# Kernel optimization log

Measured on AMD Instinct MI355X. Metric: run time of the kernel, lower is better.

## Reference

```python
import jax, jax.numpy as jnp
import numpy as np

VOCAB = 30
D_MODEL = 512
D_K = 64
D_V = 64
N_HEAD = 8
D_FF = 2048
N_LAYERS = 4
LN_EPS = 1e-5


def _make_pe(max_len, d_model):
    pos = np.arange(max_len, dtype=np.float32)[:, None]
    div = np.exp(np.arange(0, d_model, 2, dtype=np.float32) * (-np.log(10000.0) / d_model))
    pe = np.zeros((max_len, d_model), dtype=np.float32)
    pe[:, 0::2] = np.sin(pos * div)
    pe[:, 1::2] = np.cos(pos * div)
    return jnp.asarray(pe)


def setup_inputs() -> dict:
    key = jax.random.key(0)
    ks = jax.random.split(key, 16)
    B, S = 4, 2048
    s = 0.02
    inp = {
        "input_ids": jax.random.randint(ks[0], (B, S), 0, VOCAB, dtype=jnp.int64),
        "attn_mask": jax.random.randint(ks[1], (B, S), 0, 2, dtype=jnp.int64),
        "tok_embed": jax.random.normal(ks[2], (VOCAB, D_MODEL), jnp.float32) * s,
        "pe": _make_pe(S, D_MODEL),
        "Wq": jax.random.normal(ks[3], (N_LAYERS, D_MODEL, N_HEAD * D_K), jnp.float32) * s,
        "Wk": jax.random.normal(ks[4], (N_LAYERS, D_MODEL, N_HEAD * D_K), jnp.float32) * s,
        "Wv": jax.random.normal(ks[5], (N_LAYERS, D_MODEL, N_HEAD * D_V), jnp.float32) * s,
        "Wo": jax.random.normal(ks[6], (N_LAYERS, N_HEAD * D_V, D_MODEL), jnp.float32) * s,
        "ln1_g": jnp.ones((N_LAYERS, D_MODEL), jnp.float32),
        "ln1_b": jnp.zeros((N_LAYERS, D_MODEL), jnp.float32),
        "W1": jax.random.normal(ks[7], (N_LAYERS, D_MODEL, D_FF), jnp.float32) * s,
        "W2": jax.random.normal(ks[8], (N_LAYERS, D_FF, D_MODEL), jnp.float32) * s,
        "ln2_g": jnp.ones((N_LAYERS, D_MODEL), jnp.float32),
        "ln2_b": jnp.zeros((N_LAYERS, D_MODEL), jnp.float32),
    }
    return inp


def _layernorm(x, g, b):
    mu = jnp.mean(x, axis=-1, keepdims=True)
    var = jnp.mean(jnp.square(x - mu), axis=-1, keepdims=True)
    return (x - mu) * jax.lax.rsqrt(var + LN_EPS) * g + b


def reference(input_ids, attn_mask, tok_embed, pe, Wq, Wk, Wv, Wo, ln1_g, ln1_b, W1, W2, ln2_g, ln2_b):
    B, S = input_ids.shape
    x = tok_embed[input_ids] + pe[:S][None]  # [B,S,D]
    # pad mask: key positions where attn_mask==0, broadcast over heads & queries
    pad = (attn_mask == 0)[:, None, None, :]  # [B,1,1,S]
    scale = 1.0 / np.sqrt(D_K)
    for l in range(N_LAYERS):
        # multi-head self-attention
        q = (x @ Wq[l]).reshape(B, S, N_HEAD, D_K)
        k = (x @ Wk[l]).reshape(B, S, N_HEAD, D_K)
        v = (x @ Wv[l]).reshape(B, S, N_HEAD, D_V)
        scores = jnp.einsum('bqhd,bkhd->bhqk', q, k) * scale
        scores = jnp.where(pad, -1e9, scores)
        attn = jax.nn.softmax(scores, axis=-1)
        ctx = jnp.einsum('bhqk,bkhd->bqhd', attn, v).reshape(B, S, N_HEAD * D_V)
        x = _layernorm(ctx @ Wo[l] + x, ln1_g[l], ln1_b[l])
        # position-wise FFN
        h = jax.nn.relu(x @ W1[l])
        x = _layernorm(h @ W2[l] + x, ln2_g[l], ln2_b[l])
    return x
```

## Files before the change

kernel.cpp:

```cpp
#include <hip/hip_runtime.h>
#include <stdint.h>

#define S_LEN 2048
#define B_SZ 4
#define DM 512
#define NTOK (B_SZ * S_LEN)

typedef unsigned short u16;
typedef unsigned int u32;
typedef unsigned long long u64;
typedef __attribute__((ext_vector_type(8))) short short8;
typedef __attribute__((ext_vector_type(4))) float f32x4;

typedef const __attribute__((address_space(1))) u32 gq_t;
typedef __attribute__((address_space(3))) u32 lq_t;

__device__ __forceinline__ u16 f2bf(float f) {
  union { float f; u32 u; } v; v.f = f;
  return (u16)((v.u + 0x7FFFu + ((v.u >> 16) & 1u)) >> 16);
}

__device__ __forceinline__ float bf2f(u32 hi16_at_lo) {
  union { u32 u; float f; } v; v.u = hi16_at_lo;
  return v.f;
}

__device__ __forceinline__ float fexp2(float x) {
#if __has_builtin(__builtin_amdgcn_exp2f)
  return __builtin_amdgcn_exp2f(x);
#else
  return exp2f(x);
#endif
}

__device__ __forceinline__ short8 mk8(u64 a, u64 b) {
  union { u64 q[2]; short8 s; } u;
  u.q[0] = a; u.q[1] = b;
  return u.s;
}

__device__ __forceinline__ void swap32(u32& x, u32& y) {
  asm("v_permlane32_swap_b32 %0, %1" : "+v"(x), "+v"(y));
}
__device__ __forceinline__ void swap16(u32& x, u32& y, int lane) {
#if __has_builtin(__builtin_amdgcn_permlane16_swap)
  asm("v_permlane16_swap_b32 %0, %1" : "+v"(x), "+v"(y));
#else
  u32 tx = __builtin_amdgcn_ds_swizzle(x, 0x401F);
  u32 ty = __builtin_amdgcn_ds_swizzle(y, 0x401F);
  bool up = (lane & 16) != 0;
  u32 nx = up ? ty : x;
  u32 ny = up ? y : tx;
  x = nx; y = ny;
#endif
}

__global__ void embed_kernel(const int* __restrict__ ids, const float* __restrict__ te,
                             const float* __restrict__ pe, float* __restrict__ x,
                             u16* __restrict__ xb) {
  int gid = blockIdx.x * 256 + threadIdx.x;
  int tok = gid >> 7, c4 = (gid & 127) << 2;
  int s = tok & (S_LEN - 1);
  int id = ids[tok];
  const float4 a = *(const float4*)(te + (long)id * DM + c4);
  const float4 p = *(const float4*)(pe + (long)s * DM + c4);
  float4 o; o.x = a.x + p.x; o.y = a.y + p.y; o.z = a.z + p.z; o.w = a.w + p.w;
  *(float4*)(x + (long)tok * DM + c4) = o;
  uint2 pk;
  pk.x = (u32)f2bf(o.x) | ((u32)f2bf(o.y) << 16);
  pk.y = (u32)f2bf(o.z) | ((u32)f2bf(o.w) << 16);
  *(uint2*)(xb + (long)tok * DM + c4) = pk;
}

__global__ void wconv_all(const float* __restrict__ Wq, const float* __restrict__ Wk,
                          const float* __restrict__ Wv, const float* __restrict__ Wo,
                          const float* __restrict__ W1, const float* __restrict__ W2,
                          u16* __restrict__ WqkvT, u16* __restrict__ WoT,
                          u16* __restrict__ W1T, u16* __restrict__ W2T) {
  long gid = (long)blockIdx.x * 256 + threadIdx.x;
  const long SQ = 4L * 512 * 512;
  const long SF = 4L * 512 * 2048;
  const float* src; u16* dst; int K, N, ls, noff; long g2;
  if (gid < 3 * SQ) {
    int which = (int)(gid / SQ); g2 = gid % SQ;
    src = which == 0 ? Wq : which == 1 ? Wk : Wv;
    dst = WqkvT; K = 512; N = 512; ls = 1536 * 512; noff = 512 * which;
  } else if (gid < 4 * SQ) {
    g2 = gid - 3 * SQ; src = Wo; dst = WoT; K = 512; N = 512; ls = 512 * 512; noff = 0;
  } else if (gid < 4 * SQ + SF) {
    g2 = gid - 4 * SQ; src = W1; dst = W1T; K = 512; N = 2048; ls = 2048 * 512; noff = 0;
  } else {
    g2 = gid - 4 * SQ - SF; src = W2; dst = W2T; K = 2048; N = 512; ls = 512 * 2048; noff = 0;
  }
  int k = (int)(g2 % K);
  int n = (int)((g2 / K) % N);
  int l = (int)(g2 / ((long)K * N));
  dst[(long)l * ls + (long)(noff + n) * K + k] = f2bf(src[(long)l * K * N + (long)k * N + n]);
}

template <int BM, int BN, bool RELU, bool VSPLIT, bool SWAPC>
__global__ __launch_bounds__(BM * 2) void gemm_kernel(const u16* __restrict__ A,
                                                      const u16* __restrict__ BT,
                                                      void* __restrict__ Cout,
                                                      u16* __restrict__ vt,
                                                      int M, int N, int K) {
  constexpr int NI = BN / 32;
  constexpr int NW = BM / 32;
  constexpr int BRW = BN / NW;
  constexpr int LOADS = 4 + BRW / 8;
  __shared__ __align__(16) u16 a_t[2][BM * 64];
  __shared__ __align__(16) u16 b_t[2][BN * 64];
  const int tid = threadIdx.x;
  const int w = tid >> 6, lane = tid & 63;
  const int wr = w >> 1, wc = w & 1;
  const int g = lane >> 4, lr = lane & 15;
  const int l8 = lane >> 3, lch = lane & 7;
  const int gc = lch ^ l8;
  const int nwg = gridDim.x * gridDim.y;
  const int bid = blockIdx.x + gridDim.x * blockIdx.y;
  const int cpx = nwg >> 3;
  const int swz = (bid & 7) * cpx + (bid >> 3);
  const int bx = swz % gridDim.x, by = swz / gridDim.x;
  const long m0 = (long)by * BM, n0 = (long)bx * BN;
  f32x4 acc[4][NI] = {};
  const int nk = K >> 6;

  auto stage = [&](int nb, int kt) {
    const int k0 = kt << 6;
#pragma unroll
    for (int i = 0; i < 4; ++i) {
      int row = w * 32 + i * 8 + l8;
      __builtin_amdgcn_global_load_lds((gq_t*)(A + (m0 + row) * K + k0 + gc * 8),
                                       (lq_t*)&a_t[nb][(w * 4 + i) * 512], 16, 0, 0);
    }
#pragma unroll
    for (int i = 0; i < BRW / 8; ++i) {
      int row = w * BRW + i * 8 + l8;
      __builtin_amdgcn_global_load_lds((gq_t*)(BT + (n0 + row) * K + k0 + gc * 8),
                                       (lq_t*)&b_t[nb][(w * (BRW / 8) + i) * 512], 16, 0, 0);
    }
  };

  stage(0, 0);
  stage(1, 1);
  for (int kt = 0; kt < nk; ++kt) {
    const int cur = kt & 1;
    if (kt + 1 < nk) {
      if constexpr (LOADS == 6) asm volatile("s_waitcnt vmcnt(6)" ::: "memory");
      else                      asm volatile("s_waitcnt vmcnt(5)" ::: "memory");
    } else {
      asm volatile("s_waitcnt vmcnt(0)" ::: "memory");
    }
    __builtin_amdgcn_s_barrier();
    __builtin_amdgcn_sched_barrier(0);
    short8 af[2][4], bfr[2][NI];
#pragma unroll
    for (int ks = 0; ks < 2; ++ks) {
#pragma unroll
      for (int mi = 0; mi < 4; ++mi) {
        int row = wr * 64 + mi * 16 + lr;
        int byte = row * 128 + (((ks * 4 + g) ^ (row & 7)) << 4);
        af[ks][mi] = *(const short8*)((const char*)a_t[cur] + byte);
      }
#pragma unroll
      for (int ni = 0; ni < NI; ++ni) {
        int row = wc * (BN / 2) + ni * 16 + lr;
        int byte = row * 128 + (((ks * 4 + g) ^ (row & 7)) << 4);
        bfr[ks][ni] = *(const short8*)((const char*)b_t[cur] + byte);
      }
    }
    asm volatile("s_waitcnt lgkmcnt(0)" ::: "memory");
    __builtin_amdgcn_s_barrier();
    __builtin_amdgcn_sched_barrier(0);
    if (kt + 2 < nk) stage(cur, kt + 2);
#pragma unroll
    for (int ks = 0; ks < 2; ++ks)
#pragma unroll
      for (int mi = 0; mi < 4; ++mi)
#pragma unroll
        for (int ni = 0; ni < NI; ++ni) {
          if constexpr (SWAPC)
            acc[mi][ni] = __builtin_amdgcn_mfma_f32_16x16x32_bf16(bfr[ks][ni], af[ks][mi], acc[mi][ni], 0, 0, 0);
          else
            acc[mi][ni] = __builtin_amdgcn_mfma_f32_16x16x32_bf16(af[ks][mi], bfr[ks][ni], acc[mi][ni], 0, 0, 0);
        }
  }

  if constexpr (VSPLIT) {
    if (n0 >= 1024) {
#pragma unroll
      for (int mi = 0; mi < 4; ++mi)
#pragma unroll
        for (int ni = 0; ni < NI; ++ni) {
          int vc = (int)(n0 - 1024) + wc * (BN / 2) + ni * 16 + lr;
          int hh = vc >> 6, d = vc & 63;
          long tok0 = m0 + wr * 64 + mi * 16 + g * 4;
          int bb = (int)(tok0 >> 11), s0 = (int)(tok0 & 2047);
          uint2 pk;
          pk.x = (u32)f2bf(acc[mi][ni][0]) | ((u32)f2bf(acc[mi][ni][1]) << 16);
          pk.y = (u32)f2bf(acc[mi][ni][2]) | ((u32)f2bf(acc[mi][ni][3]) << 16);
          *(uint2*)(vt + (((long)bb * 8 + hh) * 64 + d) * 2048 + s0) = pk;
        }
      return;
    }
  }
  if constexpr (SWAPC) {
#pragma unroll
    for (int mi = 0; mi < 4; ++mi)
#pragma unroll
      for (int ni = 0; ni < NI; ++ni) {
        long grow = m0 + wr * 64 + mi * 16 + lr;
        long gcb = n0 + wc * (BN / 2) + ni * 16 + 4 * g;
        float v0 = acc[mi][ni][0], v1 = acc[mi][ni][1], v2 = acc[mi][ni][2], v3 = acc[mi][ni][3];
        if (RELU) {
          v0 = fmaxf(v0, 0.f); v1 = fmaxf(v1, 0.f); v2 = fmaxf(v2, 0.f); v3 = fmaxf(v3, 0.f);
        }
        uint2 pk;
        pk.x = (u32)f2bf(v0) | ((u32)f2bf(v1) << 16);
        pk.y = (u32)f2bf(v2) | ((u32)f2bf(v3) << 16);
        *(uint2*)((u16*)Cout + grow * N + gcb) = pk;
      }
  } else {
#pragma unroll
    for (int mi = 0; mi < 4; ++mi)
#pragma unroll
      for (int ni = 0; ni < NI; ++ni)
#pragma unroll
        for (int j = 0; j < 4; ++j) {
          long grow = m0 + wr * 64 + mi * 16 + g * 4 + j;
          long gcol = n0 + wc * (BN / 2) + ni * 16 + lr;
          float v = acc[mi][ni][j];
          if (RELU) v = fmaxf(v, 0.f);
          ((u16*)Cout)[grow * N + gcol] = f2bf(v);
        }
  }
}

__global__ __launch_bounds__(512) void attn_kernel(const u16* __restrict__ qkv,
                                                   const u16* __restrict__ vt,
                                                   const int* __restrict__ mask,
                                                   u16* __restrict__ ctx) {
  __shared__ __align__(16) u16 k_t[2][64 * 64];
  __shared__ __align__(16) u16 v_t[2][80 * 64];
  __shared__ __align__(16) u16 q_t[128 * 64];
  __shared__ __align__(16) float mvals[2][64];
  __shared__ __align__(16) float l_lds[128];
  const int tid = threadIdx.x;
  const int w = tid >> 6, lane = tid & 63;
  const int g = lane >> 4, lr = lane & 15;
  const int l8 = lane >> 3, lch = lane & 7;
  const int gc = lch ^ l8;
  const int b = blockIdx.z, h = blockIdx.y, q0 = blockIdx.x * 128;
  const long base = (long)b * S_LEN * 1536;
  const int qcol = h * 64, kcol = 512 + h * 64;
  const u16* vhead = vt + (((long)b * 8 + h) * 64) * 2048;
  const float SC = 0.18033688011112042f;

  auto stageKV = [&](int nb, int kb) {
    {
      int row = w * 8 + l8;
      __builtin_amdgcn_global_load_lds((gq_t*)(qkv + base + (long)(kb + row) * 1536 + kcol + gc * 8),
                                       (lq_t*)&k_t[nb][w * 512], 16, 0, 0);
    }
    {
      int row = w * 8 + l8;
      __builtin_amdgcn_global_load_lds((gq_t*)(vhead + (long)row * 2048 + kb + gc * 8),
                                       (lq_t*)&v_t[nb][w * 512], 16, 0, 0);
    }
    if (tid < 64) mvals[nb][tid] = (mask[b * S_LEN + kb + tid] == 0) ? -1e9f : 0.f;
  };

  {
    int r16 = tid >> 5;
    u32 val = (r16 == 0) ? 0x3F803F80u : 0u;
    *(u32*)((char*)v_t[0] + 64 * 128 + tid * 4) = val;
    *(u32*)((char*)v_t[1] + 64 * 128 + tid * 4) = val;
  }
#pragma unroll
  for (int i = 0; i < 2; ++i) {
    int e = i * 512 + tid;
    int row = e >> 3, ch = e & 7;
    uint4 v = *(const uint4*)(qkv + base + (long)(q0 + row) * 1536 + qcol + ch * 8);
    *(uint4*)((char*)q_t + row * 128 + ((ch ^ (row & 7)) << 4)) = v;
  }
  stageKV(0, 0);
  __syncthreads();
  short8 qf[2];
#pragma unroll
  for (int ks = 0; ks < 2; ++ks) {
    int row = w * 16 + lr;
    qf[ks] = *(const short8*)((const char*)q_t + row * 128 + (((ks * 4 + g) ^ (row & 7)) << 4));
  }

  f32x4 o[5] = {};

  for (int kt = 0; kt < S_LEN / 64; ++kt) {
    const int cur = kt & 1;
    if (kt + 1 < S_LEN / 64) stageKV(cur ^ 1, (kt + 1) * 64);

    f32x4 s[4] = {};
#pragma unroll
    for (int ks = 0; ks < 2; ++ks) {
#pragma unroll
      for (int ni = 0; ni < 4; ++ni) {
        int row = ni * 16 + lr;
        short8 kf = *(const short8*)((const char*)k_t[cur] + row * 128 + (((ks * 4 + g) ^ (row & 7)) << 4));
        s[ni] = __builtin_amdgcn_mfma_f32_16x16x32_bf16(kf, qf[ks], s[ni], 0, 0, 0);
      }
    }
    float p[4][4];
#pragma unroll
    for (int ni = 0; ni < 4; ++ni) {
      const float4 mv = *(const float4*)&mvals[cur][ni * 16 + 4 * g];
      const float mva[4] = {mv.x, mv.y, mv.z, mv.w};
#pragma unroll
      for (int r = 0; r < 4; ++r)
        p[ni][r] = fexp2(fmaf(s[ni][r], SC, mva[r]));
    }
    u32 wv[4][2];
#pragma unroll
    for (int ni = 0; ni < 4; ++ni)
#pragma unroll
      for (int pp = 0; pp < 2; ++pp)
        asm("v_cvt_pk_bf16_f32 %0, %1, %2"
            : "=v"(wv[ni][pp]) : "v"(p[ni][2 * pp]), "v"(p[ni][2 * pp + 1]));

    u32 x0 = wv[0][0], x1 = wv[0][1], y0 = wv[1][0], y1 = wv[1][1];
    swap32(x0, y0); swap32(x1, y1);
    swap16(x0, y0, lane); swap16(x1, y1, lane);
    short8 pa0 = mk8((u64)x0 | ((u64)x1 << 32), (u64)y0 | ((u64)y1 << 32));
    u32 x2 = wv[2][0], x3 = wv[2][1], y2 = wv[3][0], y3 = wv[3][1];
    swap32(x2, y2); swap32(x3, y3);
    swap16(x2, y2, lane); swap16(x3, y3, lane);
    short8 pa1 = mk8((u64)x2 | ((u64)x3 << 32), (u64)y2 | ((u64)y3 << 32));

#pragma unroll
    for (int ks2 = 0; ks2 < 2; ++ks2) {
      short8 pa = ks2 ? pa1 : pa0;
#pragma unroll
      for (int nd = 0; nd < 5; ++nd) {
        int vrow = nd * 16 + lr;
        short8 vf = *(const short8*)((const char*)v_t[cur] + vrow * 128 + (((ks2 * 4 + g) ^ (vrow & 7)) << 4));
        o[nd] = __builtin_amdgcn_mfma_f32_16x16x32_bf16(pa, vf, o[nd], 0, 0, 0);
      }
    }
    if (kt + 1 < S_LEN / 64) __syncthreads();
  }
  if (lr == 0) {
#pragma unroll
    for (int r = 0; r < 4; ++r) l_lds[w * 16 + 4 * g + r] = o[4][r];
  }
  const float4 lv = *(const float4*)&l_lds[w * 16 + 4 * g];
  const float la[4] = {lv.x, lv.y, lv.z, lv.w};
  float inv[4];
#pragma unroll
  for (int r = 0; r < 4; ++r) inv[r] = 1.f / la[r];
#pragma unroll
  for (int nd = 0; nd < 4; ++nd)
#pragma unroll
    for (int r = 0; r < 4; ++r) {
      int tok = q0 + w * 16 + 4 * g + r;
      int col = h * 64 + nd * 16 + lr;
      ctx[((long)b * S_LEN + tok) * 512 + col] = f2bf(o[nd][r] * inv[r]);
    }
}

template <bool YBF16>
__global__ __launch_bounds__(256) void ln_kernel(const void* __restrict__ yv_,
                                                 const float* __restrict__ res,
                                                 const float* __restrict__ gam,
                                                 const float* __restrict__ bet,
                                                 float* __restrict__ out,
                                                 u16* __restrict__ ob) {
  const int row = blockIdx.x, t = threadIdx.x;
  const long o0 = (long)row * DM;
  float y0, y1;
  if constexpr (YBF16) {
    u32 wbits = *(const u32*)((const u16*)yv_ + o0 + 2 * t);
    y0 = bf2f(wbits << 16);
    y1 = bf2f(wbits & 0xFFFF0000u);
  } else {
    const float2 yv = *(const float2*)((const float*)yv_ + o0 + 2 * t);
    y0 = yv.x; y1 = yv.y;
  }
  const float2 rv = *(const float2*)&res[o0 + 2 * t];
  float a0 = y0 + rv.x;
  float a1 = y1 + rv.y;
  float s1 = a0 + a1, s2 = a0 * a0 + a1 * a1;
#pragma unroll
  for (int m = 32; m >= 1; m >>= 1) {
    s1 += __shfl_xor(s1, m);
    s2 += __shfl_xor(s2, m);
  }
  __shared__ float w1[4], w2[4];
  if ((t & 63) == 0) { w1[t >> 6] = s1; w2[t >> 6] = s2; }
  __syncthreads();
  s1 = w1[0] + w1[1] + w1[2] + w1[3];
  s2 = w2[0] + w2[1] + w2[2] + w2[3];
  const float mu = s1 * (1.f / DM);
  const float rstd = rsqrtf(s2 * (1.f / DM) - mu * mu + 1e-5f);
  const float2 gv = *(const float2*)&gam[2 * t];
  const float2 bv = *(const float2*)&bet[2 * t];
  float r0 = (a0 - mu) * rstd * gv.x + bv.x;
  float r1 = (a1 - mu) * rstd * gv.y + bv.y;
  float2 ov; ov.x = r0; ov.y = r1;
  *(float2*)&out[o0 + 2 * t] = ov;
  if (ob) {
    u32 pk = (u32)f2bf(r0) | ((u32)f2bf(r1) << 16);
    *(u32*)&ob[o0 + 2 * t] = pk;
  }
}

extern "C" void kernel_launch(void* const* d_in, const int* in_sizes, int n_in,
                              void* d_out, int out_size, void* d_ws, size_t ws_size,
                              hipStream_t stream) {
  const int*   ids  = (const int*)d_in[0];
  const int*   amsk = (const int*)d_in[1];
  const float* te   = (const float*)d_in[2];
  const float* pe   = (const float*)d_in[3];
  const float* Wq   = (const float*)d_in[4];
  const float* Wk   = (const float*)d_in[5];
  const float* Wv   = (const float*)d_in[6];
  const float* Wo   = (const float*)d_in[7];
  const float* ln1g = (const float*)d_in[8];
  const float* ln1b = (const float*)d_in[9];
  const float* W1   = (const float*)d_in[10];
  const float* W2   = (const float*)d_in[11];
  const float* ln2g = (const float*)d_in[12];
  const float* ln2b = (const float*)d_in[13];
  float* out = (float*)d_out;

  char* p = (char*)d_ws;
  float* x   = (float*)p; p += (long)NTOK * DM * 4;
  u16* qkv   = (u16*)p;   p += (long)NTOK * 1536 * 2;
  u16* ctx   = (u16*)p;   p += (long)NTOK * DM * 2;
  u16* tmp   = (u16*)p;   p += (long)NTOK * DM * 4;
  u16* hb    = (u16*)p;   p += (long)NTOK * 2048 * 2;
  u16* WqkvT = (u16*)p;   p += (long)4 * 1536 * 512 * 2;
  u16* WoT   = (u16*)p;   p += (long)4 * 512 * 512 * 2;
  u16* W1T   = (u16*)p;   p += (long)4 * 2048 * 512 * 2;
  u16* W2T   = (u16*)p;   p += (long)4 * 512 * 2048 * 2;
  if ((size_t)(p - (char*)d_ws) > ws_size) return;
  u16* vt = hb;

  {
    long total = 4L * 512 * 512 * 4 + 2L * 4 * 512 * 2048;
    wconv_all<<<(int)((total + 255) / 256), 256, 0, stream>>>(
        Wq, Wk, Wv, Wo, W1, W2, WqkvT, WoT, W1T, W2T);
  }
  embed_kernel<<<NTOK * 128 / 256, 256, 0, stream>>>(ids, te, pe, x, ctx);

  for (int l = 0; l < 4; ++l) {
    gemm_kernel<256, 64, false, true, false><<<dim3(1536 / 64, NTOK / 256), 512, 0, stream>>>(
        ctx, WqkvT + (long)l * 1536 * 512, qkv, vt, NTOK, 1536, 512);
    attn_kernel<<<dim3(S_LEN / 128, 8, B_SZ), 512, 0, stream>>>(qkv, vt, amsk, ctx);
    gemm_kernel<128, 64, false, false, true><<<dim3(512 / 64, NTOK / 128), 256, 0, stream>>>(
        ctx, WoT + (long)l * 512 * 512, tmp, nullptr, NTOK, 512, 512);
    ln_kernel<true><<<NTOK, 256, 0, stream>>>(tmp, x, ln1g + l * 512, ln1b + l * 512, x, ctx);
    gemm_kernel<256, 64, true, false, true><<<dim3(2048 / 64, NTOK / 256), 512, 0, stream>>>(
        ctx, W1T + (long)l * 2048 * 512, hb, nullptr, NTOK, 2048, 512);
    gemm_kernel<128, 64, false, false, true><<<dim3(512 / 64, NTOK / 128), 256, 0, stream>>>(
        hb, W2T + (long)l * 512 * 2048, tmp, nullptr, NTOK, 512, 2048);
    ln_kernel<true><<<NTOK, 256, 0, stream>>>(tmp, x, ln2g + l * 512, ln2b + l * 512,
                                              (l == 3) ? out : x, (l == 3) ? (u16*)nullptr : ctx);
  }
}
```

Before: 662.2 us.

## Store residual stream in bf16 and tile-transpose weight conversion through LDS

The fp32 residual copy of the activations is dropped. Embedding and layernorm now write a single bf16 buffer, which serves both as the GEMM input and as the residual that layernorm reads back, so each layernorm moves less memory. Weight conversion now processes 64x64 tiles through LDS, giving coalesced float4 reads and packed writes instead of strided scalar accesses. The cost is lower residual precision, since bf16 rounding accumulates across layers.

```diff
diff --git a/kernel.cpp b/kernel.cpp
--- a/kernel.cpp
+++ b/kernel.cpp
@@ -56,19 +56,16 @@
 }
 
 __global__ void embed_kernel(const int* __restrict__ ids, const float* __restrict__ te,
-                             const float* __restrict__ pe, float* __restrict__ x,
-                             u16* __restrict__ xb) {
+                             const float* __restrict__ pe, u16* __restrict__ xb) {
   int gid = blockIdx.x * 256 + threadIdx.x;
   int tok = gid >> 7, c4 = (gid & 127) << 2;
   int s = tok & (S_LEN - 1);
   int id = ids[tok];
   const float4 a = *(const float4*)(te + (long)id * DM + c4);
   const float4 p = *(const float4*)(pe + (long)s * DM + c4);
-  float4 o; o.x = a.x + p.x; o.y = a.y + p.y; o.z = a.z + p.z; o.w = a.w + p.w;
-  *(float4*)(x + (long)tok * DM + c4) = o;
   uint2 pk;
-  pk.x = (u32)f2bf(o.x) | ((u32)f2bf(o.y) << 16);
-  pk.y = (u32)f2bf(o.z) | ((u32)f2bf(o.w) << 16);
+  pk.x = (u32)f2bf(a.x + p.x) | ((u32)f2bf(a.y + p.y) << 16);
+  pk.y = (u32)f2bf(a.z + p.z) | ((u32)f2bf(a.w + p.w) << 16);
   *(uint2*)(xb + (long)tok * DM + c4) = pk;
 }
 
@@ -77,25 +74,55 @@
                           const float* __restrict__ W1, const float* __restrict__ W2,
                           u16* __restrict__ WqkvT, u16* __restrict__ WoT,
                           u16* __restrict__ W1T, u16* __restrict__ W2T) {
-  long gid = (long)blockIdx.x * 256 + threadIdx.x;
-  const long SQ = 4L * 512 * 512;
-  const long SF = 4L * 512 * 2048;
-  const float* src; u16* dst; int K, N, ls, noff; long g2;
-  if (gid < 3 * SQ) {
-    int which = (int)(gid / SQ); g2 = gid % SQ;
-    src = which == 0 ? Wq : which == 1 ? Wk : Wv;
-    dst = WqkvT; K = 512; N = 512; ls = 1536 * 512; noff = 512 * which;
-  } else if (gid < 4 * SQ) {
-    g2 = gid - 3 * SQ; src = Wo; dst = WoT; K = 512; N = 512; ls = 512 * 512; noff = 0;
-  } else if (gid < 4 * SQ + SF) {
-    g2 = gid - 4 * SQ; src = W1; dst = W1T; K = 512; N = 2048; ls = 2048 * 512; noff = 0;
+  __shared__ u16 t_lds[64 * 65];
+  const int tile = blockIdx.x;
+  const float* src; u16* dst; int N, K, kt, nt, l;
+  if (tile < 768) {
+    int which = tile >> 8, r = tile & 255;
+    l = r >> 6; int rr = r & 63; kt = rr >> 3; nt = rr & 7;
+    src = (which == 0 ? Wq : which == 1 ? Wk : Wv) + (long)l * 512 * 512;
+    N = 512; K = 512;
+    dst = WqkvT + (long)l * 1536 * 512 + (long)(which * 512) * 512;
+  } else if (tile < 1024) {
+    int r = tile - 768;
+    l = r >> 6; int rr = r & 63; kt = rr >> 3; nt = rr & 7;
+    src = Wo + (long)l * 512 * 512; N = 512; K = 512;
+    dst = WoT + (long)l * 512 * 512;
+  } else if (tile < 2048) {
+    int r = tile - 1024;
+    l = r >> 8; int rr = r & 255; kt = rr >> 5; nt = rr & 31;
+    src = W1 + (long)l * 512 * 2048; N = 2048; K = 512;
+    dst = W1T + (long)l * 2048 * 512;
   } else {
-    g2 = gid - 4 * SQ - SF; src = W2; dst = W2T; K = 2048; N = 512; ls = 512 * 2048; noff = 0;
-  }
-  int k = (int)(g2 % K);
-  int n = (int)((g2 / K) % N);
-  int l = (int)(g2 / ((long)K * N));
-  dst[(long)l * ls + (long)(noff + n) * K + k] = f2bf(src[(long)l * K * N + (long)k * N + n]);
+    int r = tile - 2048;
+    l = r >> 8; int rr = r & 255; kt = rr >> 3; nt = rr & 7;
+    src = W2 + (long)l * 2048 * 512; N = 512; K = 2048;
+    dst = W2T + (long)l * 512 * 2048;
+  }
+  const int tr = threadIdx.x >> 4;
+  const int tc = (threadIdx.x & 15) << 2;
+#pragma unroll
+  for (int i = 0; i < 4; ++i) {
+    int k = tr + i * 16;
+    const float4 v = *(const float4*)(src + (long)(kt * 64 + k) * N + nt * 64 + tc);
+    t_lds[(tc + 0) * 65 + k] = f2bf(v.x);
+    t_lds[(tc + 1) * 65 + k] = f2bf(v.y);
+    t_lds[(tc + 2) * 65 + k] = f2bf(v.z);
+    t_lds[(tc + 3) * 65 + k] = f2bf(v.w);
+  }
+  __syncthreads();
+#pragma unroll
+  for (int i = 0; i < 4; ++i) {
+    int n = tr + i * 16;
+    u16 a0 = t_lds[n * 65 + tc + 0];
+    u16 a1 = t_lds[n * 65 + tc + 1];
+    u16 a2 = t_lds[n * 65 + tc + 2];
+    u16 a3 = t_lds[n * 65 + tc + 3];
+    uint2 pk;
+    pk.x = (u32)a0 | ((u32)a1 << 16);
+    pk.y = (u32)a2 | ((u32)a3 << 16);
+    *(uint2*)(dst + (long)(nt * 64 + n) * K + kt * 64 + tc) = pk;
+  }
 }
 
 template <int BM, int BN, bool RELU, bool VSPLIT, bool SWAPC>
@@ -365,27 +392,19 @@
     }
 }
 
-template <bool YBF16>
-__global__ __launch_bounds__(256) void ln_kernel(const void* __restrict__ yv_,
-                                                 const float* __restrict__ res,
+template <bool FINAL>
+__global__ __launch_bounds__(256) void ln_kernel(const u16* __restrict__ y,
+                                                 const u16* __restrict__ res,
                                                  const float* __restrict__ gam,
                                                  const float* __restrict__ bet,
-                                                 float* __restrict__ out,
-                                                 u16* __restrict__ ob) {
+                                                 u16* __restrict__ xout,
+                                                 float* __restrict__ outf) {
   const int row = blockIdx.x, t = threadIdx.x;
   const long o0 = (long)row * DM;
-  float y0, y1;
-  if constexpr (YBF16) {
-    u32 wbits = *(const u32*)((const u16*)yv_ + o0 + 2 * t);
-    y0 = bf2f(wbits << 16);
-    y1 = bf2f(wbits & 0xFFFF0000u);
-  } else {
-    const float2 yv = *(const float2*)((const float*)yv_ + o0 + 2 * t);
-    y0 = yv.x; y1 = yv.y;
-  }
-  const float2 rv = *(const float2*)&res[o0 + 2 * t];
-  float a0 = y0 + rv.x;
-  float a1 = y1 + rv.y;
+  const u32 yb = *(const u32*)(y + o0 + 2 * t);
+  const u32 rb = *(const u32*)(res + o0 + 2 * t);
+  float a0 = bf2f(yb << 16) + bf2f(rb << 16);
+  float a1 = bf2f(yb & 0xFFFF0000u) + bf2f(rb & 0xFFFF0000u);
   float s1 = a0 + a1, s2 = a0 * a0 + a1 * a1;
 #pragma unroll
   for (int m = 32; m >= 1; m >>= 1) {
@@ -403,11 +422,12 @@
   const float2 bv = *(const float2*)&bet[2 * t];
   float r0 = (a0 - mu) * rstd * gv.x + bv.x;
   float r1 = (a1 - mu) * rstd * gv.y + bv.y;
-  float2 ov; ov.x = r0; ov.y = r1;
-  *(float2*)&out[o0 + 2 * t] = ov;
-  if (ob) {
+  if constexpr (FINAL) {
+    float2 ov; ov.x = r0; ov.y = r1;
+    *(float2*)&outf[o0 + 2 * t] = ov;
+  } else {
     u32 pk = (u32)f2bf(r0) | ((u32)f2bf(r1) << 16);
-    *(u32*)&ob[o0 + 2 * t] = pk;
+    *(u32*)&xout[o0 + 2 * t] = pk;
   }
 }
 
@@ -431,10 +451,10 @@
   float* out = (float*)d_out;
 
   char* p = (char*)d_ws;
-  float* x   = (float*)p; p += (long)NTOK * DM * 4;
+  u16* x     = (u16*)p;   p += (long)NTOK * DM * 2;
   u16* qkv   = (u16*)p;   p += (long)NTOK * 1536 * 2;
   u16* ctx   = (u16*)p;   p += (long)NTOK * DM * 2;
-  u16* tmp   = (u16*)p;   p += (long)NTOK * DM * 4;
+  u16* tmp   = (u16*)p;   p += (long)NTOK * DM * 2;
   u16* hb    = (u16*)p;   p += (long)NTOK * 2048 * 2;
   u16* WqkvT = (u16*)p;   p += (long)4 * 1536 * 512 * 2;
   u16* WoT   = (u16*)p;   p += (long)4 * 512 * 512 * 2;
@@ -443,25 +463,23 @@
   if ((size_t)(p - (char*)d_ws) > ws_size) return;
   u16* vt = hb;
 
-  {
-    long total = 4L * 512 * 512 * 4 + 2L * 4 * 512 * 2048;
-    wconv_all<<<(int)((total + 255) / 256), 256, 0, stream>>>(
-        Wq, Wk, Wv, Wo, W1, W2, WqkvT, WoT, W1T, W2T);
-  }
-  embed_kernel<<<NTOK * 128 / 256, 256, 0, stream>>>(ids, te, pe, x, ctx);
+  wconv_all<<<3072, 256, 0, stream>>>(Wq, Wk, Wv, Wo, W1, W2, WqkvT, WoT, W1T, W2T);
+  embed_kernel<<<NTOK * 128 / 256, 256, 0, stream>>>(ids, te, pe, x);
 
   for (int l = 0; l < 4; ++l) {
     gemm_kernel<256, 64, false, true, false><<<dim3(1536 / 64, NTOK / 256), 512, 0, stream>>>(
-        ctx, WqkvT + (long)l * 1536 * 512, qkv, vt, NTOK, 1536, 512);
+        x, WqkvT + (long)l * 1536 * 512, qkv, vt, NTOK, 1536, 512);
     attn_kernel<<<dim3(S_LEN / 128, 8, B_SZ), 512, 0, stream>>>(qkv, vt, amsk, ctx);
     gemm_kernel<128, 64, false, false, true><<<dim3(512 / 64, NTOK / 128), 256, 0, stream>>>(
         ctx, WoT + (long)l * 512 * 512, tmp, nullptr, NTOK, 512, 512);
-    ln_kernel<true><<<NTOK, 256, 0, stream>>>(tmp, x, ln1g + l * 512, ln1b + l * 512, x, ctx);
+    ln_kernel<false><<<NTOK, 256, 0, stream>>>(tmp, x, ln1g + l * 512, ln1b + l * 512, x, nullptr);
     gemm_kernel<256, 64, true, false, true><<<dim3(2048 / 64, NTOK / 256), 512, 0, stream>>>(
-        ctx, W1T + (long)l * 2048 * 512, hb, nullptr, NTOK, 2048, 512);
+        x, W1T + (long)l * 2048 * 512, hb, nullptr, NTOK, 2048, 512);
     gemm_kernel<128, 64, false, false, true><<<dim3(512 / 64, NTOK / 128), 256, 0, stream>>>(
         hb, W2T + (long)l * 512 * 2048, tmp, nullptr, NTOK, 512, 2048);
-    ln_kernel<true><<<NTOK, 256, 0, stream>>>(tmp, x, ln2g + l * 512, ln2b + l * 512,
-                                              (l == 3) ? out : x, (l == 3) ? (u16*)nullptr : ctx);
-  }
-}
+    if (l == 3)
+      ln_kernel<true><<<NTOK, 256, 0, stream>>>(tmp, x, ln2g + l * 512, ln2b + l * 512, nullptr, out);
+    else
+      ln_kernel<false><<<NTOK, 256, 0, stream>>>(tmp, x, ln2g + l * 512, ln2b + l * 512, x, nullptr);
+  }
+}
```

Result: faster. 599.7 us (-9.4%).
